# Kernel optimization log

Measured on AMD Instinct MI355X. Metric: run time of the kernel, lower is better.

## Reference

```python
import jax, jax.numpy as jnp
import numpy as np

T = 1024      # number of timesteps
B = 32768     # number of independent regions / batch elements
STEP = 0.5    # fixed Euler step size (self.step in the torch module)


def setup_inputs() -> dict:
    key = jax.random.key(0)
    k1, k2, k3, k4 = jax.random.split(key, 4)
    return {
        "initial": jax.random.uniform(k1, (4, B), dtype=jnp.float32),  # [S0,E0,I0,R0]
        "beta": jax.random.uniform(k2, (1,), dtype=jnp.float32),
        "gamma": jax.random.uniform(k3, (1,), dtype=jnp.float32),
        "sigma": jax.random.uniform(k4, (1,), dtype=jnp.float32),
        "t": T,
    }


def reference(initial, beta, gamma, sigma, t):
    # Faithful Euler SEIR stepping: each update uses the *previous* step's
    # values of all four compartments (matches the torch indexing with [n]).
    step = jnp.float32(STEP)
    b, g, s = beta[0], gamma[0], sigma[0]
    S0, E0, I0, R0 = initial[0], initial[1], initial[2], initial[3]  # each (B,)

    def body(carry, _):
        S, E, I, R = carry
        Sn = S - b * S * I * step
        En = E + (b * S * I - s * E) * step
        In = I + (s * E - g * I) * step
        Rn = R + g * I * step
        new = (Sn, En, In, Rn)
        return new, new

    _, traj = jax.lax.scan(body, (S0, E0, I0, R0), None, length=t - 1)
    # Prepend initial state; torch cats time-major per compartment -> (t*B,)
    Ss = jnp.concatenate([S0[None], traj[0]], axis=0).reshape(-1)
    Es = jnp.concatenate([E0[None], traj[1]], axis=0).reshape(-1)
    Is = jnp.concatenate([I0[None], traj[2]], axis=0).reshape(-1)
    Rs = jnp.concatenate([R0[None], traj[3]], axis=0).reshape(-1)
    return jnp.stack([Ss, Es, Is, Rs], axis=1)  # (t*B, 4)
```

## Files before the change

kernel.cpp:

```cpp
#include <hip/hip_runtime.h>

#define T_STEPS 1024
#define B_ELEMS 32768
#define STEP 0.5f

typedef float f32x4 __attribute__((ext_vector_type(4)));

__global__ __launch_bounds__(64) void seir_euler_kernel(
    const float* __restrict__ initial,
    const float* __restrict__ beta,
    const float* __restrict__ gamma,
    const float* __restrict__ sigma,
    f32x4* __restrict__ out)
{
    constexpr int B = B_ELEMS;
    const int b = blockIdx.x * 64 + threadIdx.x;

    const float bb = beta[0];
    const float gg = gamma[0];
    const float ss = sigma[0];

    float S = initial[0 * B + b];
    float E = initial[1 * B + b];
    float I = initial[2 * B + b];
    float R = initial[3 * B + b];

    size_t idx = (size_t)b;
#pragma unroll 8
    for (int n = 0; n < T_STEPS; ++n, idx += B) {
        f32x4 v = {S, E, I, R};
        __builtin_nontemporal_store(v, &out[idx]);
        float bSI = bb * S * I;
        float sE  = ss * E;
        float gI  = gg * I;
        float Sn = S - bSI * STEP;
        float En = E + (bSI - sE) * STEP;
        float In = I + (sE - gI) * STEP;
        float Rn = R + gI * STEP;
        S = Sn; E = En; I = In; R = Rn;
    }
}

extern "C" void kernel_launch(void* const* d_in, const int* in_sizes, int n_in,
                              void* d_out, int out_size, void* d_ws, size_t ws_size,
                              hipStream_t stream)
{
    const float* initial = (const float*)d_in[0];
    const float* beta    = (const float*)d_in[1];
    const float* gamma   = (const float*)d_in[2];
    const float* sigma   = (const float*)d_in[3];
    f32x4* out = (f32x4*)d_out;

    const int block = 64;
    const int grid = B_ELEMS / block;
    seir_euler_kernel<<<grid, block, 0, stream>>>(initial, beta, gamma, sigma, out);
}
```

Measured before the change: 96.50 us.

## Split Euler recurrence into checkpoint pass and parallel per-segment store pass

A first kernel runs the serial SEIR recurrence per element and writes the state at 8 evenly spaced time checkpoints into workspace. A second kernel, with 8x as many threads, restarts from each checkpoint and writes its 128-step segment of the trajectory. The aim is more waves in flight during the store-bound output write than one thread per batch element can give. The cost is an extra serial compute pass, a second launch and a small workspace round trip. It falls back to the original kernel if workspace is too small.

```diff
diff --git a/kernel.cpp b/kernel.cpp
--- a/kernel.cpp
+++ b/kernel.cpp
@@ -2,9 +2,82 @@
 
 #define T_STEPS 1024
 #define B_ELEMS 32768
+#define K_CKPT 8
+#define NS (T_STEPS / K_CKPT)
 #define STEP 0.5f
 
 typedef float f32x4 __attribute__((ext_vector_type(4)));
+
+#define ADVANCE()                                  \
+    do {                                           \
+        float bSI = bb * S * I;                    \
+        float sE  = ss * E;                        \
+        float gI  = gg * I;                        \
+        float Sn = S - bSI * STEP;                 \
+        float En = E + (bSI - sE) * STEP;          \
+        float In = I + (sE - gI) * STEP;           \
+        float Rn = R + gI * STEP;                  \
+        S = Sn; E = En; I = In; R = Rn;            \
+    } while (0)
+
+__global__ __launch_bounds__(64) void seir_ckpt_kernel(
+    const float* __restrict__ initial,
+    const float* __restrict__ beta,
+    const float* __restrict__ gamma,
+    const float* __restrict__ sigma,
+    float* __restrict__ ws)
+{
+    constexpr int B = B_ELEMS;
+    const int b = blockIdx.x * 64 + threadIdx.x;
+
+    const float bb = beta[0];
+    const float gg = gamma[0];
+    const float ss = sigma[0];
+
+    float S = initial[0 * B + b];
+    float E = initial[1 * B + b];
+    float I = initial[2 * B + b];
+    float R = initial[3 * B + b];
+
+    for (int k = 0; k < K_CKPT; ++k) {
+        ws[(k * 4 + 0) * B + b] = S;
+        ws[(k * 4 + 1) * B + b] = E;
+        ws[(k * 4 + 2) * B + b] = I;
+        ws[(k * 4 + 3) * B + b] = R;
+        if (k < K_CKPT - 1) {
+            for (int i = 0; i < NS; ++i) ADVANCE();
+        }
+    }
+}
+
+__global__ __launch_bounds__(256) void seir_store_kernel(
+    const float* __restrict__ beta,
+    const float* __restrict__ gamma,
+    const float* __restrict__ sigma,
+    const float* __restrict__ ws,
+    f32x4* __restrict__ out)
+{
+    constexpr int B = B_ELEMS;
+    constexpr int BLOCKS_PER_K = B / 256;
+    const int k = blockIdx.x / BLOCKS_PER_K;
+    const int b = (blockIdx.x % BLOCKS_PER_K) * 256 + threadIdx.x;
+
+    const float bb = beta[0];
+    const float gg = gamma[0];
+    const float ss = sigma[0];
+
+    float S = ws[(k * 4 + 0) * B + b];
+    float E = ws[(k * 4 + 1) * B + b];
+    float I = ws[(k * 4 + 2) * B + b];
+    float R = ws[(k * 4 + 3) * B + b];
+
+    size_t idx = (size_t)k * NS * B + b;
+    for (int n = 0; n < NS; ++n, idx += B) {
+        f32x4 v = {S, E, I, R};
+        __builtin_nontemporal_store(v, &out[idx]);
+        ADVANCE();
+    }
+}
 
 __global__ __launch_bounds__(64) void seir_euler_kernel(
     const float* __restrict__ initial,
@@ -26,18 +99,10 @@
     float R = initial[3 * B + b];
 
     size_t idx = (size_t)b;
-#pragma unroll 8
     for (int n = 0; n < T_STEPS; ++n, idx += B) {
         f32x4 v = {S, E, I, R};
         __builtin_nontemporal_store(v, &out[idx]);
-        float bSI = bb * S * I;
-        float sE  = ss * E;
-        float gI  = gg * I;
-        float Sn = S - bSI * STEP;
-        float En = E + (bSI - sE) * STEP;
-        float In = I + (sE - gI) * STEP;
-        float Rn = R + gI * STEP;
-        S = Sn; E = En; I = In; R = Rn;
+        ADVANCE();
     }
 }
 
@@ -51,7 +116,13 @@
     const float* sigma   = (const float*)d_in[3];
     f32x4* out = (f32x4*)d_out;
 
-    const int block = 64;
-    const int grid = B_ELEMS / block;
-    seir_euler_kernel<<<grid, block, 0, stream>>>(initial, beta, gamma, sigma, out);
+    const size_t ws_needed = (size_t)K_CKPT * 4 * B_ELEMS * sizeof(float);
+    if (ws_size >= ws_needed) {
+        float* ws = (float*)d_ws;
+        seir_ckpt_kernel<<<B_ELEMS / 64, 64, 0, stream>>>(initial, beta, gamma, sigma, ws);
+        dim3 grid2((B_ELEMS / 256) * K_CKPT);
+        seir_store_kernel<<<grid2, 256, 0, stream>>>(beta, gamma, sigma, ws, out);
+    } else {
+        seir_euler_kernel<<<B_ELEMS / 64, 64, 0, stream>>>(initial, beta, gamma, sigma, out);
+    }
 }
```

Result: slower. 121.4 us (+25.8%).
